# Optimization experiments

Hardware: AMD Instinct MI355X
Metric: run time of the kernel (lower is better)

Reference implementation:

```python
import jax, jax.numpy as jnp
import numpy as np

HIDDEN = 192
NDIM = 3
N_NODES = 262144
BATCH = 8
N_SUPER = 2048
DEG = 16
N_EDGES = BATCH * N_SUPER * DEG  # 262144
MAX_WAVELENGTH = 10000.0


def sincos_embed(coords):
    # ContinuousSincosEmbed: dim=192, ndim=3 -> 64 dims per coord (32 sin + 32 cos), no padding
    d_per = HIDDEN // NDIM  # 64
    omega = 1.0 / MAX_WAVELENGTH ** (jnp.arange(0, d_per, 2, dtype=jnp.float32) / d_per)  # [32]
    out = coords[:, :, None] * omega[None, None, :]            # [N, ndim, 32]
    emb = jnp.concatenate([jnp.sin(out), jnp.cos(out)], -1)    # [N, ndim, 64]
    return emb.reshape(coords.shape[0], HIDDEN)                # [N, 192]


def _xavier(key, fan_in, fan_out):
    bound = np.sqrt(6.0 / (fan_in + fan_out)).astype(np.float32)
    return jax.random.uniform(key, (fan_in, fan_out), jnp.float32, -bound, bound)


def setup_inputs() -> dict:
    key = jax.random.key(0)
    k = jax.random.split(key, 8)
    mesh_pos = jax.random.normal(k[0], (N_NODES, NDIM), jnp.float32)
    # edges grouped by sorted dst (segment_csr precondition); every supernode appears DEG times
    dst = jnp.repeat(jnp.arange(BATCH * N_SUPER, dtype=jnp.int32), DEG)          # [E]
    src = jax.random.randint(k[1], (N_EDGES,), 0, N_NODES, dtype=jnp.int32)      # [E]
    mesh_edges = jnp.stack([dst, src], axis=1)                                   # [E, 2]
    batch_idx = jnp.repeat(jnp.arange(BATCH, dtype=jnp.int32), N_NODES // BATCH)
    return {
        "mesh_pos": mesh_pos,
        "mesh_edges": mesh_edges,
        "batch_idx": batch_idx,
        "W1": _xavier(k[2], 2 * HIDDEN, 2 * HIDDEN), "b1": jnp.zeros((2 * HIDDEN,), jnp.float32),
        "W2": _xavier(k[3], 2 * HIDDEN, HIDDEN),     "b2": jnp.zeros((HIDDEN,), jnp.float32),
        "W3": _xavier(k[4], HIDDEN, HIDDEN),         "b3": jnp.zeros((HIDDEN,), jnp.float32),
    }


def reference(mesh_pos, mesh_edges, batch_idx, W1, b1, W2, b2, W3, b3):
    x = sincos_embed(mesh_pos)                       # [N, H]
    dst_idx = mesh_edges[:, 0]
    src_idx = mesh_edges[:, 1]
    h = jnp.concatenate([x[src_idx], x[dst_idx]], axis=1)        # [E, 2H]
    h = jax.nn.gelu(h @ W1 + b1, approximate=False)
    h = jax.nn.gelu(h @ W2 + b2, approximate=False)
    h = h @ W3 + b3                                              # [E, H]
    num_segments = BATCH * N_SUPER  # = number of unique dst by construction
    sums = jax.ops.segment_sum(h, dst_idx, num_segments=num_segments)
    counts = jax.ops.segment_sum(jnp.ones((h.shape[0],), h.dtype), dst_idx,
                                 num_segments=num_segments)
    mean = sums / jnp.maximum(counts, 1.0)[:, None]              # segment_csr mean
    return mean.reshape(BATCH, N_SUPER, HIDDEN)
```

## Files before the change

### kernel.cpp

```cpp
#include <hip/hip_runtime.h>

#define HID    192
#define HID2   384
#define NEDGES 262144
#define MB     64
#define NBLK   (NEDGES / MB)

#define ALD   200
#define LDA   392
#define DSTE_OFF 12800
#define DSTC_OFF 25088
#define SMEM_ELEMS 26624

typedef __bf16 bf16;
typedef __bf16 bv8  __attribute__((ext_vector_type(8)));
typedef float f32x4 __attribute__((ext_vector_type(4)));

__device__ __forceinline__ float gelu_fast(float x) {
    float x2 = x * x;
    float u2 = 1.5957691216057308f * x * __builtin_fmaf(0.044715f, x2, 1.0f);
    float e  = __expf(u2);
    float inv = __builtin_amdgcn_rcpf(e + 1.0f);
    return __builtin_fmaf(-x, inv, x);
}

__global__ void wprep_kernel(const float* __restrict__ W1, const float* __restrict__ W2,
                             const float* __restrict__ W3,
                             bf16* __restrict__ W1T, bf16* __restrict__ W2T,
                             bf16* __restrict__ W3T) {
    int idx = blockIdx.x * 256 + threadIdx.x;
    if (idx < 147456) {
        int n = idx / 384, k = idx - n * 384;
        W1T[idx] = (bf16)W1[k * 384 + n];
    } else if (idx < 221184) {
        int j = idx - 147456;
        int n = j / 384, k = j - n * 384;
        W2T[j] = (bf16)W2[k * 192 + n];
    } else if (idx < 258048) {
        int j = idx - 221184;
        int n = j / 192, k = j - n * 192;
        W3T[j] = (bf16)W3[k * 192 + n];
    }
}

__global__ __launch_bounds__(256, 3)
void fused_mlp_kernel(const float* __restrict__ pos, const int* __restrict__ edges,
                      const bf16* __restrict__ W1T, const float* __restrict__ b1,
                      const bf16* __restrict__ W2T, const float* __restrict__ b2,
                      const bf16* __restrict__ W3T, const float* __restrict__ b3,
                      float* __restrict__ out) {
    __shared__ __align__(16) bf16 smem[SMEM_ELEMS];
    const int tid  = threadIdx.x;
    const int wave = tid >> 6;
    const int lane = tid & 63;
    const int quad = lane >> 4;
    const int l15  = lane & 15;
    const int blk  = blockIdx.x;

    {
        const int r    = tid >> 2;
        const int part = tid & 3;
        const int e    = blk * MB + r;
        const int node = edges[2 * e + 1];
        const float p0 = pos[node * 3 + 0];
        const float p1 = pos[node * 3 + 1];
        const float p2 = pos[node * 3 + 2];
        bf16* ldst = smem + r * ALD + part * 48;
        #pragma unroll
        for (int g = 0; g < 6; ++g) {
            const int t0    = part * 48 + g * 8;
            const int dim   = t0 >> 6;
            const int isCos = t0 & 32;
            const int f0    = t0 & 31;
            const float pv  = (dim == 0) ? p0 : ((dim == 1) ? p1 : p2);
            float om = exp2f(-0.4152410118609203f * (float)f0);
            bv8 v;
            #pragma unroll
            for (int j = 0; j < 8; ++j) {
                const float x = pv * om;
                v[j] = (bf16)(isCos ? __cosf(x) : __sinf(x));
                om *= 0.74989420933245582f;
            }
            *reinterpret_cast<bv8*>(ldst + g * 8) = v;
        }
    }
    if (tid < 192) {
        const int s    = tid / 48;
        const int c0   = (tid - s * 48) * 4;
        const int node = edges[2 * (blk * MB + s * 16)];
        const int dim  = c0 >> 6;
        const int isCos = c0 & 32;
        const int f0   = c0 & 31;
        const float pv = pos[node * 3 + dim];
        float om = exp2f(-0.4152410118609203f * (float)f0);
        bf16 v[4];
        #pragma unroll
        for (int j = 0; j < 4; ++j) {
            const float x = pv * om;
            v[j] = (bf16)(isCos ? __cosf(x) : __sinf(x));
            om *= 0.74989420933245582f;
        }
        *reinterpret_cast<uint2*>(smem + DSTE_OFF + s * ALD + c0) = *reinterpret_cast<uint2*>(v);
    }
    __syncthreads();

    const f32x4 fz = {0.f, 0.f, 0.f, 0.f};

    {
        f32x4 accd[6];
        #pragma unroll
        for (int nn = 0; nn < 6; ++nn) accd[nn] = fz;
        const bf16* wbase = W1T + (size_t)(wave * 96 + l15) * HID2 + 192 + quad * 8;
        for (int kt = 0; kt < 6; ++kt) {
            bv8 a = *reinterpret_cast<const bv8*>(smem + DSTE_OFF + l15 * ALD + kt * 32 + quad * 8);
            #pragma unroll
            for (int nn = 0; nn < 6; ++nn) {
                bv8 b = *reinterpret_cast<const bv8*>(wbase + (size_t)nn * 16 * HID2 + kt * 32);
                accd[nn] = __builtin_amdgcn_mfma_f32_16x16x32_bf16(a, b, accd[nn], 0, 0, 0);
            }
        }
        if (quad == 0) {
            #pragma unroll
            for (int nn = 0; nn < 6; ++nn) {
                const int col = wave * 96 + nn * 16 + l15;
                #pragma unroll
                for (int r = 0; r < 4; ++r)
                    smem[DSTC_OFF + r * HID2 + col] = (bf16)accd[nn][r];
            }
        }
    }

    f32x4 acc1[4][6];
    #pragma unroll
    for (int m = 0; m < 4; ++m)
        #pragma unroll
        for (int nn = 0; nn < 6; ++nn) acc1[m][nn] = fz;
    {
        const bf16* wbase = W1T + (size_t)(wave * 96 + l15) * HID2 + quad * 8;
        for (int kt = 0; kt < 6; ++kt) {
            const bf16* abase = smem + l15 * ALD + kt * 32 + quad * 8;
            bv8 a[4];
            #pragma unroll
            for (int m = 0; m < 4; ++m)
                a[m] = *reinterpret_cast<const bv8*>(abase + m * 16 * ALD);
            #pragma unroll
            for (int nn = 0; nn < 6; ++nn) {
                bv8 b = *reinterpret_cast<const bv8*>(wbase + (size_t)nn * 16 * HID2 + kt * 32);
                #pragma unroll
                for (int m = 0; m < 4; ++m)
                    acc1[m][nn] = __builtin_amdgcn_mfma_f32_16x16x32_bf16(a[m], b, acc1[m][nn], 0, 0, 0);
            }
        }
    }
    __syncthreads();

    #pragma unroll
    for (int nn = 0; nn < 6; ++nn) {
        const int col   = wave * 96 + nn * 16 + l15;
        const float bia = b1[col];
        #pragma unroll
        for (int m = 0; m < 4; ++m) {
            const float dc = (float)smem[DSTC_OFF + m * HID2 + col];
            #pragma unroll
            for (int r = 0; r < 4; ++r)
                smem[(m * 16 + quad * 4 + r) * LDA + col] = (bf16)gelu_fast(acc1[m][nn][r] + dc + bia);
        }
    }
    __syncthreads();

    f32x4 acc2[4][3];
    #pragma unroll
    for (int m = 0; m < 4; ++m)
        #pragma unroll
        for (int nn = 0; nn < 3; ++nn) acc2[m][nn] = fz;
    {
        const bf16* wbase = W2T + (size_t)(wave * 48 + l15) * HID2 + quad * 8;
        for (int kt = 0; kt < 12; ++kt) {
            const bf16* abase = smem + l15 * LDA + kt * 32 + quad * 8;
            bv8 a[4];
            #pragma unroll
            for (int m = 0; m < 4; ++m)
                a[m] = *reinterpret_cast<const bv8*>(abase + m * 16 * LDA);
            #pragma unroll
            for (int nn = 0; nn < 3; ++nn) {
                bv8 b = *reinterpret_cast<const bv8*>(wbase + (size_t)nn * 16 * HID2 + kt * 32);
                #pragma unroll
                for (int m = 0; m < 4; ++m)
                    acc2[m][nn] = __builtin_amdgcn_mfma_f32_16x16x32_bf16(a[m], b, acc2[m][nn], 0, 0, 0);
            }
        }
    }
    __syncthreads();

    #pragma unroll
    for (int nn = 0; nn < 3; ++nn) {
        const int col   = wave * 48 + nn * 16 + l15;
        const float bia = b2[col];
        #pragma unroll
        for (int m = 0; m < 4; ++m) {
            float s = gelu_fast(acc2[m][nn][0] + bia) + gelu_fast(acc2[m][nn][1] + bia)
                    + gelu_fast(acc2[m][nn][2] + bia) + gelu_fast(acc2[m][nn][3] + bia);
            s += __shfl_xor(s, 16);
            s += __shfl_xor(s, 32);
            if (quad == 0)
                smem[m * ALD + col] = (bf16)(s * 0.0625f);
        }
    }
    __syncthreads();

    {
        f32x4 acc3[3];
        #pragma unroll
        for (int nn = 0; nn < 3; ++nn) acc3[nn] = fz;
        const bf16* wbase = W3T + (size_t)(wave * 48 + l15) * HID + quad * 8;
        for (int kt = 0; kt < 6; ++kt) {
            bv8 a = *reinterpret_cast<const bv8*>(smem + l15 * ALD + kt * 32 + quad * 8);
            #pragma unroll
            for (int nn = 0; nn < 3; ++nn) {
                bv8 b = *reinterpret_cast<const bv8*>(wbase + (size_t)nn * 16 * HID + kt * 32);
                acc3[nn] = __builtin_amdgcn_mfma_f32_16x16x32_bf16(a, b, acc3[nn], 0, 0, 0);
            }
        }
        if (quad == 0) {
            #pragma unroll
            for (int nn = 0; nn < 3; ++nn) {
                const int col   = wave * 48 + nn * 16 + l15;
                const float bia = b3[col];
                #pragma unroll
                for (int r = 0; r < 4; ++r)
                    out[(size_t)(blk * 4 + r) * HID + col] = acc3[nn][r] + bia;
            }
        }
    }
}

extern "C" void kernel_launch(void* const* d_in, const int* in_sizes, int n_in,
                              void* d_out, int out_size, void* d_ws, size_t ws_size,
                              hipStream_t stream) {
    const float* mesh_pos = (const float*)d_in[0];
    const int*   edges    = (const int*)  d_in[1];
    const float* W1 = (const float*)d_in[3];
    const float* b1 = (const float*)d_in[4];
    const float* W2 = (const float*)d_in[5];
    const float* b2 = (const float*)d_in[6];
    const float* W3 = (const float*)d_in[7];
    const float* b3 = (const float*)d_in[8];
    float* out = (float*)d_out;

    bf16* W1T = (bf16*)d_ws;
    bf16* W2T = W1T + 147456;
    bf16* W3T = W2T + 73728;

    wprep_kernel<<<(258048 + 255) / 256, 256, 0, stream>>>(W1, W2, W3, W1T, W2T, W3T);
    fused_mlp_kernel<<<NBLK, 256, 0, stream>>>(mesh_pos, edges, W1T, b1, W2T, b2, W3T, b3, out);
}
```

Baseline: 327.9 us.

## Use 512-thread blocks with swapped-operand MFMA tiling and padded LDS layouts

Doubles the block to 8 waves and splits each GEMM stage across them. Layer 1 swaps the operands so the weights form the A side and edges form the B side, which allows packed 4-wide bf16 stores of the activations. Layer 2 is split across two row groups of 4 waves each, and the LDS strides are re-padded (408, 208) to cut bank conflicts. The aim is more waves per CU for latency hiding, at the cost of more barrier synchronisation and half the waves sitting idle during the small layer-3 GEMM.

```diff
diff --git a/kernel.cpp b/kernel.cpp
--- a/kernel.cpp
+++ b/kernel.cpp
@@ -7,13 +7,17 @@
 #define NBLK   (NEDGES / MB)
 
 #define ALD   200
-#define LDA   392
-#define DSTE_OFF 12800
-#define DSTC_OFF 25088
-#define SMEM_ELEMS 26624
+#define DLD   200
+#define H1LD  408
+#define MLD   208
+#define DSTE  12800
+#define DSTC  26112
+#define MH2   26112
+#define SMEM_ELEMS 27648
 
 typedef __bf16 bf16;
-typedef __bf16 bv8  __attribute__((ext_vector_type(8)));
+typedef __bf16 bv8 __attribute__((ext_vector_type(8)));
+typedef __bf16 bv4 __attribute__((ext_vector_type(4)));
 typedef float f32x4 __attribute__((ext_vector_type(4)));
 
 __device__ __forceinline__ float gelu_fast(float x) {
@@ -43,7 +47,7 @@
     }
 }
 
-__global__ __launch_bounds__(256, 3)
+__global__ __launch_bounds__(512, 4)
 void fused_mlp_kernel(const float* __restrict__ pos, const int* __restrict__ edges,
                       const bf16* __restrict__ W1T, const float* __restrict__ b1,
                       const bf16* __restrict__ W2T, const float* __restrict__ b2,
@@ -51,24 +55,24 @@
                       float* __restrict__ out) {
     __shared__ __align__(16) bf16 smem[SMEM_ELEMS];
     const int tid  = threadIdx.x;
-    const int wave = tid >> 6;
+    const int w    = tid >> 6;
     const int lane = tid & 63;
     const int quad = lane >> 4;
     const int l15  = lane & 15;
     const int blk  = blockIdx.x;
 
     {
-        const int r    = tid >> 2;
-        const int part = tid & 3;
+        const int r    = tid >> 3;
+        const int part = tid & 7;
         const int e    = blk * MB + r;
         const int node = edges[2 * e + 1];
         const float p0 = pos[node * 3 + 0];
         const float p1 = pos[node * 3 + 1];
         const float p2 = pos[node * 3 + 2];
-        bf16* ldst = smem + r * ALD + part * 48;
-        #pragma unroll
-        for (int g = 0; g < 6; ++g) {
-            const int t0    = part * 48 + g * 8;
+        bf16* ldst = smem + r * ALD + part * 24;
+        #pragma unroll
+        for (int g = 0; g < 3; ++g) {
+            const int t0    = part * 24 + g * 8;
             const int dim   = t0 >> 6;
             const int isCos = t0 & 32;
             const int f0    = t0 & 31;
@@ -93,142 +97,148 @@
         const int f0   = c0 & 31;
         const float pv = pos[node * 3 + dim];
         float om = exp2f(-0.4152410118609203f * (float)f0);
-        bf16 v[4];
+        bv4 v;
         #pragma unroll
         for (int j = 0; j < 4; ++j) {
             const float x = pv * om;
             v[j] = (bf16)(isCos ? __cosf(x) : __sinf(x));
             om *= 0.74989420933245582f;
         }
-        *reinterpret_cast<uint2*>(smem + DSTE_OFF + s * ALD + c0) = *reinterpret_cast<uint2*>(v);
+        *reinterpret_cast<bv4*>(smem + DSTE + s * DLD + c0) = v;
     }
     __syncthreads();
 
     const f32x4 fz = {0.f, 0.f, 0.f, 0.f};
 
     {
-        f32x4 accd[6];
-        #pragma unroll
-        for (int nn = 0; nn < 6; ++nn) accd[nn] = fz;
-        const bf16* wbase = W1T + (size_t)(wave * 96 + l15) * HID2 + 192 + quad * 8;
+        f32x4 accd[3];
+        #pragma unroll
+        for (int mc = 0; mc < 3; ++mc) accd[mc] = fz;
+        const bf16* wb = W1T + (size_t)(w * 48 + l15) * HID2 + 192 + quad * 8;
+        const bf16* db = smem + DSTE + (l15 & 3) * DLD + quad * 8;
         for (int kt = 0; kt < 6; ++kt) {
-            bv8 a = *reinterpret_cast<const bv8*>(smem + DSTE_OFF + l15 * ALD + kt * 32 + quad * 8);
-            #pragma unroll
-            for (int nn = 0; nn < 6; ++nn) {
-                bv8 b = *reinterpret_cast<const bv8*>(wbase + (size_t)nn * 16 * HID2 + kt * 32);
-                accd[nn] = __builtin_amdgcn_mfma_f32_16x16x32_bf16(a, b, accd[nn], 0, 0, 0);
-            }
-        }
-        if (quad == 0) {
-            #pragma unroll
-            for (int nn = 0; nn < 6; ++nn) {
-                const int col = wave * 96 + nn * 16 + l15;
+            bv8 bfrag = *reinterpret_cast<const bv8*>(db + kt * 32);
+            #pragma unroll
+            for (int mc = 0; mc < 3; ++mc) {
+                bv8 afrag = *reinterpret_cast<const bv8*>(wb + mc * 16 * HID2 + kt * 32);
+                accd[mc] = __builtin_amdgcn_mfma_f32_16x16x32_bf16(afrag, bfrag, accd[mc], 0, 0, 0);
+            }
+        }
+        if (l15 < 4) {
+            #pragma unroll
+            for (int mc = 0; mc < 3; ++mc) {
+                bv4 pk;
+                #pragma unroll
+                for (int r = 0; r < 4; ++r) pk[r] = (bf16)accd[mc][r];
+                *reinterpret_cast<bv4*>(smem + DSTC + l15 * HID2 + w * 48 + mc * 16 + quad * 4) = pk;
+            }
+        }
+    }
+
+    f32x4 acc1[3][4];
+    #pragma unroll
+    for (int mc = 0; mc < 3; ++mc)
+        #pragma unroll
+        for (int ne = 0; ne < 4; ++ne) acc1[mc][ne] = fz;
+    {
+        const bf16* wb = W1T + (size_t)(w * 48 + l15) * HID2 + quad * 8;
+        const bf16* xb = smem + l15 * ALD + quad * 8;
+        for (int kt = 0; kt < 6; ++kt) {
+            bv8 x[4];
+            #pragma unroll
+            for (int ne = 0; ne < 4; ++ne)
+                x[ne] = *reinterpret_cast<const bv8*>(xb + ne * 16 * ALD + kt * 32);
+            #pragma unroll
+            for (int mc = 0; mc < 3; ++mc) {
+                bv8 a = *reinterpret_cast<const bv8*>(wb + mc * 16 * HID2 + kt * 32);
+                #pragma unroll
+                for (int ne = 0; ne < 4; ++ne)
+                    acc1[mc][ne] = __builtin_amdgcn_mfma_f32_16x16x32_bf16(a, x[ne], acc1[mc][ne], 0, 0, 0);
+            }
+        }
+    }
+    __syncthreads();
+
+    {
+        const int cb = w * 48 + quad * 4;
+        #pragma unroll
+        for (int mc = 0; mc < 3; ++mc) {
+            f32x4 bia = *reinterpret_cast<const f32x4*>(b1 + cb + mc * 16);
+            #pragma unroll
+            for (int ne = 0; ne < 4; ++ne) {
+                bv4 dc = *reinterpret_cast<const bv4*>(smem + DSTC + ne * HID2 + cb + mc * 16);
+                bv4 o;
                 #pragma unroll
                 for (int r = 0; r < 4; ++r)
-                    smem[DSTC_OFF + r * HID2 + col] = (bf16)accd[nn][r];
-            }
-        }
-    }
-
-    f32x4 acc1[4][6];
+                    o[r] = (bf16)gelu_fast(acc1[mc][ne][r] + (float)dc[r] + bia[r]);
+                *reinterpret_cast<bv4*>(smem + (ne * 16 + l15) * H1LD + cb + mc * 16) = o;
+            }
+        }
+    }
+    __syncthreads();
+
+    const int mgrp = w >> 2;
+    const int ncb  = (w & 3) * 3;
+    f32x4 acc2[2][3];
     #pragma unroll
-    for (int m = 0; m < 4; ++m)
-        #pragma unroll
-        for (int nn = 0; nn < 6; ++nn) acc1[m][nn] = fz;
-    {
-        const bf16* wbase = W1T + (size_t)(wave * 96 + l15) * HID2 + quad * 8;
-        for (int kt = 0; kt < 6; ++kt) {
-            const bf16* abase = smem + l15 * ALD + kt * 32 + quad * 8;
-            bv8 a[4];
-            #pragma unroll
-            for (int m = 0; m < 4; ++m)
-                a[m] = *reinterpret_cast<const bv8*>(abase + m * 16 * ALD);
-            #pragma unroll
-            for (int nn = 0; nn < 6; ++nn) {
-                bv8 b = *reinterpret_cast<const bv8*>(wbase + (size_t)nn * 16 * HID2 + kt * 32);
-                #pragma unroll
-                for (int m = 0; m < 4; ++m)
-                    acc1[m][nn] = __builtin_amdgcn_mfma_f32_16x16x32_bf16(a[m], b, acc1[m][nn], 0, 0, 0);
-            }
-        }
-    }
-    __syncthreads();
-
+    for (int m = 0; m < 2; ++m)
+        #pragma unroll
+        for (int nc = 0; nc < 3; ++nc) acc2[m][nc] = fz;
+    {
+        const bf16* hb = smem + (mgrp * 32 + l15) * H1LD + quad * 8;
+        const bf16* wb = W2T + (size_t)(ncb * 16 + l15) * HID2 + quad * 8;
+        for (int kt = 0; kt < 12; ++kt) {
+            bv8 h[2];
+            #pragma unroll
+            for (int m = 0; m < 2; ++m)
+                h[m] = *reinterpret_cast<const bv8*>(hb + m * 16 * H1LD + kt * 32);
+            #pragma unroll
+            for (int nc = 0; nc < 3; ++nc) {
+                bv8 b = *reinterpret_cast<const bv8*>(wb + nc * 16 * HID2 + kt * 32);
+                #pragma unroll
+                for (int m = 0; m < 2; ++m)
+                    acc2[m][nc] = __builtin_amdgcn_mfma_f32_16x16x32_bf16(h[m], b, acc2[m][nc], 0, 0, 0);
+            }
+        }
+    }
     #pragma unroll
-    for (int nn = 0; nn < 6; ++nn) {
-        const int col   = wave * 96 + nn * 16 + l15;
-        const float bia = b1[col];
-        #pragma unroll
-        for (int m = 0; m < 4; ++m) {
-            const float dc = (float)smem[DSTC_OFF + m * HID2 + col];
-            #pragma unroll
-            for (int r = 0; r < 4; ++r)
-                smem[(m * 16 + quad * 4 + r) * LDA + col] = (bf16)gelu_fast(acc1[m][nn][r] + dc + bia);
-        }
-    }
-    __syncthreads();
-
-    f32x4 acc2[4][3];
-    #pragma unroll
-    for (int m = 0; m < 4; ++m)
-        #pragma unroll
-        for (int nn = 0; nn < 3; ++nn) acc2[m][nn] = fz;
-    {
-        const bf16* wbase = W2T + (size_t)(wave * 48 + l15) * HID2 + quad * 8;
-        for (int kt = 0; kt < 12; ++kt) {
-            const bf16* abase = smem + l15 * LDA + kt * 32 + quad * 8;
-            bv8 a[4];
-            #pragma unroll
-            for (int m = 0; m < 4; ++m)
-                a[m] = *reinterpret_cast<const bv8*>(abase + m * 16 * LDA);
-            #pragma unroll
-            for (int nn = 0; nn < 3; ++nn) {
-                bv8 b = *reinterpret_cast<const bv8*>(wbase + (size_t)nn * 16 * HID2 + kt * 32);
-                #pragma unroll
-                for (int m = 0; m < 4; ++m)
-                    acc2[m][nn] = __builtin_amdgcn_mfma_f32_16x16x32_bf16(a[m], b, acc2[m][nn], 0, 0, 0);
-            }
-        }
-    }
-    __syncthreads();
-
-    #pragma unroll
-    for (int nn = 0; nn < 3; ++nn) {
-        const int col   = wave * 48 + nn * 16 + l15;
-        const float bia = b2[col];
-        #pragma unroll
-        for (int m = 0; m < 4; ++m) {
-            float s = gelu_fast(acc2[m][nn][0] + bia) + gelu_fast(acc2[m][nn][1] + bia)
-                    + gelu_fast(acc2[m][nn][2] + bia) + gelu_fast(acc2[m][nn][3] + bia);
+    for (int nc = 0; nc < 3; ++nc) {
+        const int colv = (ncb + nc) * 16 + l15;
+        const float bia = b2[colv];
+        #pragma unroll
+        for (int m = 0; m < 2; ++m) {
+            float s = gelu_fast(acc2[m][nc][0] + bia) + gelu_fast(acc2[m][nc][1] + bia)
+                    + gelu_fast(acc2[m][nc][2] + bia) + gelu_fast(acc2[m][nc][3] + bia);
             s += __shfl_xor(s, 16);
             s += __shfl_xor(s, 32);
             if (quad == 0)
-                smem[m * ALD + col] = (bf16)(s * 0.0625f);
-        }
-    }
-    __syncthreads();
-
-    {
+                smem[MH2 + (mgrp * 2 + m) * MLD + colv] = (bf16)(s * 0.0625f);
+        }
+    }
+    __syncthreads();
+
+    if (w < 4) {
         f32x4 acc3[3];
         #pragma unroll
-        for (int nn = 0; nn < 3; ++nn) acc3[nn] = fz;
-        const bf16* wbase = W3T + (size_t)(wave * 48 + l15) * HID + quad * 8;
+        for (int nc = 0; nc < 3; ++nc) acc3[nc] = fz;
+        const bf16* ab = smem + MH2 + (l15 & 3) * MLD + quad * 8;
+        const bf16* wb = W3T + (size_t)(w * 48 + l15) * HID + quad * 8;
         for (int kt = 0; kt < 6; ++kt) {
-            bv8 a = *reinterpret_cast<const bv8*>(smem + l15 * ALD + kt * 32 + quad * 8);
-            #pragma unroll
-            for (int nn = 0; nn < 3; ++nn) {
-                bv8 b = *reinterpret_cast<const bv8*>(wbase + (size_t)nn * 16 * HID + kt * 32);
-                acc3[nn] = __builtin_amdgcn_mfma_f32_16x16x32_bf16(a, b, acc3[nn], 0, 0, 0);
+            bv8 a = *reinterpret_cast<const bv8*>(ab + kt * 32);
+            #pragma unroll
+            for (int nc = 0; nc < 3; ++nc) {
+                bv8 b = *reinterpret_cast<const bv8*>(wb + nc * 16 * HID + kt * 32);
+                acc3[nc] = __builtin_amdgcn_mfma_f32_16x16x32_bf16(a, b, acc3[nc], 0, 0, 0);
             }
         }
         if (quad == 0) {
             #pragma unroll
-            for (int nn = 0; nn < 3; ++nn) {
-                const int col   = wave * 48 + nn * 16 + l15;
+            for (int nc = 0; nc < 3; ++nc) {
+                const int col   = (w * 3 + nc) * 16 + l15;
                 const float bia = b3[col];
                 #pragma unroll
                 for (int r = 0; r < 4; ++r)
-                    out[(size_t)(blk * 4 + r) * HID + col] = acc3[nn][r] + bia;
+                    out[(size_t)(blk * 4 + r) * HID + col] = acc3[nc][r] + bia;
             }
         }
     }
@@ -252,5 +262,5 @@
     bf16* W3T = W2T + 73728;
 
     wprep_kernel<<<(258048 + 255) / 256, 256, 0, stream>>>(W1, W2, W3, W1T, W2T, W3T);
-    fused_mlp_kernel<<<NBLK, 256, 0, stream>>>(mesh_pos, edges, W1T, b1, W2T, b2, W3T, b3, out);
-}
+    fused_mlp_kernel<<<NBLK, 512, 0, stream>>>(mesh_pos, edges, W1T, b1, W2T, b2, W3T, b3, out);
+}
```

Measured after the change: 379.6 us. +15.8%, slower.
